# Kernel optimization log

Hardware: AMD Instinct MI355X
Metric: run time of the kernel (lower is better)

The kernel has to match this reference:

```python
import jax, jax.numpy as jnp
import numpy as np

EPS = 1e-5

def _layer_norm(x, gamma, beta):
    mu = jnp.mean(x, axis=-1, keepdims=True)
    var = jnp.var(x, axis=-1, keepdims=True)
    return (x - mu) * jax.lax.rsqrt(var + EPS) * gamma + beta

def setup_inputs() -> dict:
    key = jax.random.key(0)
    ks = jax.random.split(key, 4)
    B, T, D, H = 16, 2048, 1024, 1024
    s_in = 1.0 / np.sqrt(D)
    return {
        "x": jax.random.normal(ks[0], (B, T, D), dtype=jnp.float32),
        "c": jnp.zeros((B, H), dtype=jnp.float32),
        "W_lt": jax.random.uniform(ks[1], (H, D), jnp.float32, -s_in, s_in),
        "W_g": jax.random.uniform(ks[2], (2 * H, D), jnp.float32, -s_in, s_in),
        "b_g": jnp.zeros((2 * H,), dtype=jnp.float32),
        "gamma_g": jnp.ones((2 * H,), dtype=jnp.float32),
        "beta_g": jnp.zeros((2 * H,), dtype=jnp.float32),
        "gamma_a": jnp.ones((H,), dtype=jnp.float32),
        "beta_a": jnp.zeros((H,), dtype=jnp.float32),
    }

def reference(x, c, W_lt, W_g, b_g, gamma_g, beta_g, gamma_a, beta_a):
    H = W_lt.shape[0]
    # x: [B,T,D]
    x_tilde = jnp.einsum("btd,hd->bth", x, W_lt)            # [B,T,H]
    gate = jax.nn.sigmoid(_layer_norm(jnp.einsum("btd,gd->btg", x, W_g) + b_g, gamma_g, beta_g))
    f = gate[:, :, :H]                                        # forget gate [B,T,H]
    r = gate[:, :, H:]                                        # reset gate  [B,T,H]
    new_data = (1.0 - f) * x_tilde

    def step(c_prev, ft_nd):
        f_t, nd_t = ft_nd
        c_t = f_t * c_prev + nd_t
        return c_t, c_t

    # scan over time: move T to leading axis
    c_final, all_c = jax.lax.scan(step, c, (jnp.swapaxes(f, 0, 1), jnp.swapaxes(new_data, 0, 1)))
    all_c = jnp.swapaxes(all_c, 0, 1)                         # [B,T,H]
    h = r * jax.nn.sigmoid(_layer_norm(all_c, gamma_a, beta_a)) + (1.0 - r) * x
    return (h, c_final)
```

## Files before the change

### kernel.cpp

```cpp
#include <hip/hip_runtime.h>
#include <stdint.h>

typedef unsigned short u16;
typedef u16 us8 __attribute__((ext_vector_type(8)));
typedef uint32_t u32x8 __attribute__((ext_vector_type(8)));
typedef __bf16 bf16x8 __attribute__((ext_vector_type(8)));
typedef float f32x4 __attribute__((ext_vector_type(4)));

#define BB 16
#define TT 2048
#define HH 1024
#define MM 32768
#define NN 3072
#define KK 1024
#define NT 16

__device__ __forceinline__ float b2f(u16 u) {
    union { uint32_t i; float f; } v; v.i = ((uint32_t)u) << 16; return v.f;
}
__device__ __forceinline__ u16 f2b(float f) {
    union { uint32_t i; float f; } v; v.f = f;
    uint32_t r = v.i + 0x7fffu + ((v.i >> 16) & 1u);
    return (u16)(r >> 16);
}
__device__ __forceinline__ float sigm(float z) {
    return 1.f / (1.f + __expf(-z));
}
__device__ __forceinline__ void load_lds16(const u16* g, u16* l) {
    __builtin_amdgcn_global_load_lds(
        (const __attribute__((address_space(1))) void*)g,
        (__attribute__((address_space(3))) void*)l, 16, 0, 0);
}
__device__ __forceinline__ f32x4 mf(bf16x8 a, bf16x8 b, f32x4 c) {
    return __builtin_amdgcn_mfma_f32_16x16x32_bf16(a, b, c, 0, 0, 0);
}
#define MEMBAR() asm volatile("" ::: "memory")

__global__ __launch_bounds__(256) void k_cvt(const float* __restrict__ x,
                                             const float* __restrict__ wlt,
                                             const float* __restrict__ wg,
                                             u16* __restrict__ xb,
                                             u16* __restrict__ wb) {
    long i = (long)(blockIdx.x * 256 + threadIdx.x) * 8;
    const float* s;
    u16* o;
    if (i < 33554432L) { s = x + i; o = xb + i; }
    else {
        long j = i - 33554432L;
        s = (j < 1048576L) ? (wlt + j) : (wg + (j - 1048576L));
        o = wb + j;
    }
    float4 a = *(const float4*)(s);
    float4 b = *(const float4*)(s + 4);
    us8 r;
    r[0] = f2b(a.x); r[1] = f2b(a.y); r[2] = f2b(a.z); r[3] = f2b(a.w);
    r[4] = f2b(b.x); r[5] = f2b(b.y); r[6] = f2b(b.z); r[7] = f2b(b.w);
    *(us8*)o = r;
}

__global__ __launch_bounds__(512, 2) void k_gemm(const u16* __restrict__ A,
                                                 const u16* __restrict__ W,
                                                 u16* __restrict__ Y) {
    __shared__ u16 As[2 * 16384];
    __shared__ u16 Bs[2 * 16384];
    const int tid = threadIdx.x;
    const int lane = tid & 63;
    const int w = tid >> 6;
    const int wm = w >> 2;
    const int wn = w & 3;
    const int q = lane >> 4;
    const int l16 = lane & 15;

    const unsigned bid = blockIdx.y * 12u + blockIdx.x;
    const unsigned sw = (bid & 7u) * 192u + (bid >> 3);
    const int by = sw / 12u;
    const int bx = sw % 12u;

    const int slog = ((tid & 7) ^ ((tid >> 3) & 7)) << 3;
    const u16* aS = A + (size_t)(by * 256 + (tid >> 3)) * KK + slog;
    const u16* bS = W + (size_t)(bx * 256 + ((tid >> 8) << 6) + ((tid >> 3) & 31)) * KK + slog;
    u16* aD = As + w * 512;
    u16* bD = Bs + w * 512;

    load_lds16(aS,                aD);
    load_lds16(aS + 128 * KK,     aD + 4096);
    load_lds16(aS + 64 * KK,      aD + 8192);
    load_lds16(aS + 192 * KK,     aD + 12288);
    load_lds16(bS,                bD);
    load_lds16(bS + 128 * KK,     bD + 4096);
    load_lds16(bS + 32 * KK,      bD + 8192);
    load_lds16(bS + 160 * KK,     bD + 12288);
    load_lds16(aS + 64,           aD + 16384);
    load_lds16(aS + 64 + 128*KK,  aD + 16384 + 4096);
    load_lds16(aS + 64 + 64*KK,   aD + 16384 + 8192);
    load_lds16(aS + 64 + 192*KK,  aD + 16384 + 12288);
    load_lds16(bS + 64,           bD + 16384);
    load_lds16(bS + 64 + 128*KK,  bD + 16384 + 4096);
    load_lds16(bS + 64 + 32*KK,   bD + 16384 + 8192);
    load_lds16(bS + 64 + 160*KK,  bD + 16384 + 12288);

    const int key = l16 & 7;
    const int sA0 = ((q ^ key) << 3);
    const int sA1 = (((q ^ key) ^ 4) << 3);
    const int aB0 = wm * 4096 + l16 * 64 + sA0;
    const int aB1 = wm * 4096 + l16 * 64 + sA1;
    const int bB0 = wn * 2048 + l16 * 64 + sA0;
    const int bB1 = wn * 2048 + l16 * 64 + sA1;

    f32x4 zero = {0.f, 0.f, 0.f, 0.f};
    f32x4 acc[8][4];
#pragma unroll
    for (int i = 0; i < 8; ++i)
#pragma unroll
        for (int j = 0; j < 4; ++j) acc[i][j] = zero;
    bf16x8 aX[4], aY[4], bLo[4], bHi[4];

    asm volatile("s_waitcnt vmcnt(8)" ::: "memory");
    __builtin_amdgcn_sched_barrier(0);
    __builtin_amdgcn_s_barrier();
    MEMBAR();

    for (int kt = 0; kt < NT - 1; ++kt) {
        const int cb = (kt & 1) << 14;
        const int kc = (kt + 2) << 6;
        const bool st = (kt < NT - 2);
#pragma unroll
        for (int i = 0; i < 4; ++i) {
            aX[i] = *(const bf16x8*)&As[cb + i * 1024 + aB0];
            aY[i] = *(const bf16x8*)&As[cb + i * 1024 + aB1];
        }
        bLo[0] = *(const bf16x8*)&Bs[cb + bB0];
        bLo[1] = *(const bf16x8*)&Bs[cb + bB1];
        bLo[2] = *(const bf16x8*)&Bs[cb + 1024 + bB0];
        bLo[3] = *(const bf16x8*)&Bs[cb + 1024 + bB1];
        asm volatile("s_waitcnt lgkmcnt(8)" ::: "memory");
        __builtin_amdgcn_sched_barrier(0);
        __builtin_amdgcn_s_barrier();
        asm volatile("s_waitcnt lgkmcnt(0)" ::: "memory");
        __builtin_amdgcn_sched_barrier(0);
        __builtin_amdgcn_s_setprio(1);
#pragma unroll
        for (int i = 0; i < 4; ++i) {
            acc[i][0] = mf(aX[i], bLo[0], acc[i][0]);
            acc[i][0] = mf(aY[i], bLo[1], acc[i][0]);
            acc[i][1] = mf(aX[i], bLo[2], acc[i][1]);
            acc[i][1] = mf(aY[i], bLo[3], acc[i][1]);
        }
        __builtin_amdgcn_s_setprio(0);
        MEMBAR();
        __builtin_amdgcn_s_barrier();
        MEMBAR();
        bHi[0] = *(const bf16x8*)&Bs[cb + 8192 + bB0];
        bHi[1] = *(const bf16x8*)&Bs[cb + 8192 + bB1];
        bHi[2] = *(const bf16x8*)&Bs[cb + 8192 + 1024 + bB0];
        bHi[3] = *(const bf16x8*)&Bs[cb + 8192 + 1024 + bB1];
        if (st) {
            load_lds16(aS + kc,            aD + cb);
            load_lds16(aS + kc + 128*KK,   aD + cb + 4096);
            load_lds16(bS + kc,            bD + cb);
            load_lds16(bS + kc + 128*KK,   bD + cb + 4096);
        }
        __builtin_amdgcn_sched_barrier(0);
        __builtin_amdgcn_s_barrier();
        asm volatile("s_waitcnt lgkmcnt(0)" ::: "memory");
        __builtin_amdgcn_sched_barrier(0);
        __builtin_amdgcn_s_setprio(1);
#pragma unroll
        for (int i = 0; i < 4; ++i) {
            acc[i][2] = mf(aX[i], bHi[0], acc[i][2]);
            acc[i][2] = mf(aY[i], bHi[1], acc[i][2]);
            acc[i][3] = mf(aX[i], bHi[2], acc[i][3]);
            acc[i][3] = mf(aY[i], bHi[3], acc[i][3]);
        }
        __builtin_amdgcn_s_setprio(0);
        MEMBAR();
        __builtin_amdgcn_s_barrier();
        MEMBAR();
#pragma unroll
        for (int i = 0; i < 4; ++i) {
            aX[i] = *(const bf16x8*)&As[cb + 8192 + i * 1024 + aB0];
            aY[i] = *(const bf16x8*)&As[cb + 8192 + i * 1024 + aB1];
        }
        if (st) {
            load_lds16(bS + kc + 32*KK,    bD + cb + 8192);
            load_lds16(bS + kc + 160*KK,   bD + cb + 12288);
        }
        __builtin_amdgcn_sched_barrier(0);
        __builtin_amdgcn_s_barrier();
        asm volatile("s_waitcnt lgkmcnt(0)" ::: "memory");
        __builtin_amdgcn_sched_barrier(0);
        __builtin_amdgcn_s_setprio(1);
#pragma unroll
        for (int i = 0; i < 4; ++i) {
            acc[4 + i][0] = mf(aX[i], bLo[0], acc[4 + i][0]);
            acc[4 + i][0] = mf(aY[i], bLo[1], acc[4 + i][0]);
            acc[4 + i][1] = mf(aX[i], bLo[2], acc[4 + i][1]);
            acc[4 + i][1] = mf(aY[i], bLo[3], acc[4 + i][1]);
        }
        __builtin_amdgcn_s_setprio(0);
        MEMBAR();
        __builtin_amdgcn_s_barrier();
        MEMBAR();
        if (st) {
            load_lds16(aS + kc + 64*KK,    aD + cb + 8192);
            load_lds16(aS + kc + 192*KK,   aD + cb + 12288);
        }
        __builtin_amdgcn_sched_barrier(0);
        __builtin_amdgcn_s_barrier();
        __builtin_amdgcn_s_setprio(1);
#pragma unroll
        for (int i = 0; i < 4; ++i) {
            acc[4 + i][2] = mf(aX[i], bHi[0], acc[4 + i][2]);
            acc[4 + i][2] = mf(aY[i], bHi[1], acc[4 + i][2]);
            acc[4 + i][3] = mf(aX[i], bHi[2], acc[4 + i][3]);
            acc[4 + i][3] = mf(aY[i], bHi[3], acc[4 + i][3]);
        }
        __builtin_amdgcn_s_setprio(0);
        if (st) { asm volatile("s_waitcnt vmcnt(8)" ::: "memory"); }
        else    { asm volatile("s_waitcnt vmcnt(0)" ::: "memory"); }
        __builtin_amdgcn_sched_barrier(0);
        __builtin_amdgcn_s_barrier();
        MEMBAR();
    }

    {
        const int cb = 16384;
#pragma unroll
        for (int i = 0; i < 4; ++i) {
            aX[i] = *(const bf16x8*)&As[cb + i * 1024 + aB0];
            aY[i] = *(const bf16x8*)&As[cb + i * 1024 + aB1];
        }
        bLo[0] = *(const bf16x8*)&Bs[cb + bB0];
        bLo[1] = *(const bf16x8*)&Bs[cb + bB1];
        bLo[2] = *(const bf16x8*)&Bs[cb + 1024 + bB0];
        bLo[3] = *(const bf16x8*)&Bs[cb + 1024 + bB1];
        bHi[0] = *(const bf16x8*)&Bs[cb + 8192 + bB0];
        bHi[1] = *(const bf16x8*)&Bs[cb + 8192 + bB1];
        bHi[2] = *(const bf16x8*)&Bs[cb + 8192 + 1024 + bB0];
        bHi[3] = *(const bf16x8*)&Bs[cb + 8192 + 1024 + bB1];
#pragma unroll
        for (int i = 0; i < 4; ++i) {
            acc[i][0] = mf(aX[i], bLo[0], acc[i][0]);
            acc[i][0] = mf(aY[i], bLo[1], acc[i][0]);
            acc[i][1] = mf(aX[i], bLo[2], acc[i][1]);
            acc[i][1] = mf(aY[i], bLo[3], acc[i][1]);
            acc[i][2] = mf(aX[i], bHi[0], acc[i][2]);
            acc[i][2] = mf(aY[i], bHi[1], acc[i][2]);
            acc[i][3] = mf(aX[i], bHi[2], acc[i][3]);
            acc[i][3] = mf(aY[i], bHi[3], acc[i][3]);
        }
#pragma unroll
        for (int i = 0; i < 4; ++i) {
            aX[i] = *(const bf16x8*)&As[cb + 8192 + i * 1024 + aB0];
            aY[i] = *(const bf16x8*)&As[cb + 8192 + i * 1024 + aB1];
        }
#pragma unroll
        for (int i = 0; i < 4; ++i) {
            acc[4 + i][0] = mf(aX[i], bLo[0], acc[4 + i][0]);
            acc[4 + i][0] = mf(aY[i], bLo[1], acc[4 + i][0]);
            acc[4 + i][1] = mf(aX[i], bLo[2], acc[4 + i][1]);
            acc[4 + i][1] = mf(aY[i], bLo[3], acc[4 + i][1]);
            acc[4 + i][2] = mf(aX[i], bHi[0], acc[4 + i][2]);
            acc[4 + i][2] = mf(aY[i], bHi[1], acc[4 + i][2]);
            acc[4 + i][3] = mf(aX[i], bHi[2], acc[4 + i][3]);
            acc[4 + i][3] = mf(aY[i], bHi[3], acc[4 + i][3]);
        }
    }

#pragma unroll
    for (int fm = 0; fm < 8; ++fm) {
#pragma unroll
        for (int rg = 0; rg < 4; ++rg) {
            const int row = by * 256 + wm * 128 + fm * 16 + q * 4 + rg;
            u16* yp = Y + (size_t)row * NN + bx * 256 + wn * 64 + l16;
#pragma unroll
            for (int fn = 0; fn < 4; ++fn) yp[fn * 16] = f2b(acc[fm][fn][rg]);
        }
    }
}

__global__ __launch_bounds__(256) void k_lnsig(const u16* __restrict__ Y,
                                               const float* __restrict__ bg,
                                               const float* __restrict__ gg,
                                               const float* __restrict__ bt,
                                               uint32_t* __restrict__ FN,
                                               u16* __restrict__ R) {
    const int row = blockIdx.x;
    const int t = threadIdx.x;
    const u16* yr = Y + (size_t)row * 3072;
    us8 gv = *(const us8*)(yr + 1024 + t * 8);
    us8 xt;
    if (t < 128) xt = *(const us8*)(yr + t * 8);
    float z[8];
    float s = 0.f, s2 = 0.f;
#pragma unroll
    for (int k = 0; k < 8; k++) {
        z[k] = b2f(gv[k]) + bg[t * 8 + k];
        s += z[k];
        s2 += z[k] * z[k];
    }
#pragma unroll
    for (int m = 1; m < 64; m <<= 1) {
        s += __shfl_xor(s, m);
        s2 += __shfl_xor(s2, m);
    }
    __shared__ float red[8];
    if ((t & 63) == 0) { red[t >> 6] = s; red[(t >> 6) + 4] = s2; }
    asm volatile("s_waitcnt lgkmcnt(0)" ::: "memory");
    __builtin_amdgcn_sched_barrier(0);
    __builtin_amdgcn_s_barrier();
    MEMBAR();
    s = red[0] + red[1] + red[2] + red[3];
    s2 = red[4] + red[5] + red[6] + red[7];
    const float mu = s * (1.f / 2048.f);
    const float inv = rsqrtf(s2 * (1.f / 2048.f) - mu * mu + 1e-5f);
    float gate[8];
#pragma unroll
    for (int k = 0; k < 8; k++)
        gate[k] = sigm((z[k] - mu) * inv * gg[t * 8 + k] + bt[t * 8 + k]);
    if (t < 128) {
        u32x8 fn;
#pragma unroll
        for (int k = 0; k < 8; k++) {
            u16 fb = f2b(gate[k]);
            u16 nb = f2b((1.f - gate[k]) * b2f(xt[k]));
            fn[k] = (uint32_t)fb | ((uint32_t)nb << 16);
        }
        *(u32x8*)(FN + (size_t)row * 1024 + t * 8) = fn;
    } else {
        us8 ro;
#pragma unroll
        for (int k = 0; k < 8; k++) ro[k] = f2b(gate[k]);
        *(us8*)(R + (size_t)row * 1024 + (t - 128) * 8) = ro;
    }
}

__global__ __launch_bounds__(256) void k_scan1(const uint32_t* __restrict__ FN,
                                               float2* __restrict__ agg) {
    int u = blockIdx.x * 256 + threadIdx.x;
    int h4 = u & 255;
    int chunk = (u >> 8) & 31;
    int b = u >> 13;
    size_t base = (size_t)(b * 2048 + chunk * 64) * 1024 + h4 * 4;
    float F0 = 1.f, N0 = 0.f, F1 = 1.f, N1 = 0.f;
    float F2 = 1.f, N2 = 0.f, F3 = 1.f, N3 = 0.f;
#pragma unroll 8
    for (int i = 0; i < 64; i++) {
        uint4 v = *(const uint4*)(FN + base + (size_t)i * 1024);
        float f0 = b2f((u16)(v.x & 0xffffu)), n0 = b2f((u16)(v.x >> 16));
        float f1 = b2f((u16)(v.y & 0xffffu)), n1 = b2f((u16)(v.y >> 16));
        float f2 = b2f((u16)(v.z & 0xffffu)), n2 = b2f((u16)(v.z >> 16));
        float f3 = b2f((u16)(v.w & 0xffffu)), n3 = b2f((u16)(v.w >> 16));
        N0 = fmaf(f0, N0, n0); F0 *= f0;
        N1 = fmaf(f1, N1, n1); F1 *= f1;
        N2 = fmaf(f2, N2, n2); F2 *= f2;
        N3 = fmaf(f3, N3, n3); F3 *= f3;
    }
    size_t oi = (size_t)(b * 32 + chunk) * 1024 + h4 * 4;
    float4 oA = {F0, N0, F1, N1};
    float4 oB = {F2, N2, F3, N3};
    *(float4*)&agg[oi] = oA;
    *(float4*)&agg[oi + 2] = oB;
}

#define SOUT_STEP(fnv, rvv, xvv, ro, p)                                        \
    {                                                                          \
        c0 = fmaf(b2f((u16)((fnv).x & 0xffffu)), c0, b2f((u16)((fnv).x >> 16)));\
        c1 = fmaf(b2f((u16)((fnv).y & 0xffffu)), c1, b2f((u16)((fnv).y >> 16)));\
        float s = c0 + c1, s2 = c0 * c0 + c1 * c1;                             \
        _Pragma("unroll")                                                      \
        for (int m = 1; m < 64; m <<= 1) {                                     \
            s += __shfl_xor(s, m);                                             \
            s2 += __shfl_xor(s2, m);                                           \
        }                                                                      \
        if (lane == 0) red[p][w] = make_float2(s, s2);                         \
        asm volatile("s_waitcnt lgkmcnt(0)" ::: "memory");                     \
        __builtin_amdgcn_sched_barrier(0);                                     \
        __builtin_amdgcn_s_barrier();                                          \
        MEMBAR();                                                              \
        s = 0.f; s2 = 0.f;                                                     \
        _Pragma("unroll")                                                      \
        for (int k = 0; k < 8; k++) { float2 v = red[p][k]; s += v.x; s2 += v.y; } \
        const float mu = s * (1.f / 1024.f);                                   \
        const float inv = rsqrtf(s2 * (1.f / 1024.f) - mu * mu + 1e-5f);       \
        const float sg0 = sigm((c0 - mu) * inv * g0 + be0);                    \
        const float sg1 = sigm((c1 - mu) * inv * g1 + be1);                    \
        const float r0 = b2f((u16)((rvv) & 0xffffu)), r1 = b2f((u16)((rvv) >> 16)); \
        const float x0 = b2f((u16)((xvv) & 0xffffu)), x1 = b2f((u16)((xvv) >> 16)); \
        float2 ho = {r0 * sg0 + (1.f - r0) * x0, r1 * sg1 + (1.f - r1) * x1};  \
        *(float2*)(out + (ro)) = ho;                                           \
    }

__global__ __launch_bounds__(512) void k_scanout(const uint32_t* __restrict__ FN,
                                                 const float2* __restrict__ agg,
                                                 const float* __restrict__ cin,
                                                 const u16* __restrict__ R,
                                                 const u16* __restrict__ xb,
                                                 const float* __restrict__ ga,
                                                 const float* __restrict__ ba,
                                                 float* __restrict__ out,
                                                 float* __restrict__ cfin) {
    __shared__ float2 red[2][8];
    const int t = threadIdx.x;
    const int b = blockIdx.x >> 5, chunk = blockIdx.x & 31;
    const int h = t * 2;
    const int w = t >> 6, lane = t & 63;

    float2 cp = *(const float2*)&cin[b * 1024 + h];
    float c0 = cp.x, c1 = cp.y;
    for (int k = 0; k < chunk; ++k) {
        float4 a4 = *(const float4*)&agg[(size_t)(b * 32 + k) * 1024 + h];
        c0 = fmaf(a4.x, c0, a4.y);
        c1 = fmaf(a4.z, c1, a4.w);
    }

    const float g0 = ga[h], g1 = ga[h + 1];
    const float be0 = ba[h], be1 = ba[h + 1];
    const size_t base = (size_t)(b * 2048 + chunk * 64) * 1024 + h;

    uint2 fnA = *(const uint2*)(FN + base);
    uint32_t rvA = *(const uint32_t*)(R + base);
    uint32_t xvA = *(const uint32_t*)(xb + base);
    uint2 fnB = *(const uint2*)(FN + base + 1024);
    uint32_t rvB = *(const uint32_t*)(R + base + 1024);
    uint32_t xvB = *(const uint32_t*)(xb + base + 1024);

    for (int ii = 0; ii < 32; ++ii) {
        const size_t ro0 = base + (size_t)(2 * ii) * 1024;
        {
            uint2 fn = fnA; uint32_t rv = rvA, xv = xvA;
            if (ii < 31) {
                const size_t rn = ro0 + 2048;
                fnA = *(const uint2*)(FN + rn);
                rvA = *(const uint32_t*)(R + rn);
                xvA = *(const uint32_t*)(xb + rn);
            }
            SOUT_STEP(fn, rv, xv, ro0, 0)
        }
        {
            uint2 fn = fnB; uint32_t rv = rvB, xv = xvB;
            if (ii < 31) {
                const size_t rn = ro0 + 3072;
                fnB = *(const uint2*)(FN + rn);
                rvB = *(const uint32_t*)(R + rn);
                xvB = *(const uint32_t*)(xb + rn);
            }
            SOUT_STEP(fn, rv, xv, ro0 + 1024, 1)
        }
    }
    if (chunk == 31) *(float2*)(cfin + b * 1024 + h) = make_float2(c0, c1);
}

extern "C" void kernel_launch(void* const* d_in, const int* in_sizes, int n_in,
                              void* d_out, int out_size, void* d_ws, size_t ws_size,
                              hipStream_t stream) {
    const float* x   = (const float*)d_in[0];
    const float* c0  = (const float*)d_in[1];
    const float* wlt = (const float*)d_in[2];
    const float* wg  = (const float*)d_in[3];
    const float* bg  = (const float*)d_in[4];
    const float* gg  = (const float*)d_in[5];
    const float* btg = (const float*)d_in[6];
    const float* ga  = (const float*)d_in[7];
    const float* ba  = (const float*)d_in[8];
    float* out = (float*)d_out;

    char* ws = (char*)d_ws;
    u16* xb      = (u16*)(ws);
    u16* wb      = (u16*)(ws + 67108864);
    u16* y       = (u16*)(ws + 73400320);
    uint32_t* FN = (uint32_t*)(ws + 274726912);
    u16* R       = (u16*)(ws + 408944640);
    float2* agg  = (float2*)(ws + 476053504);

    k_cvt<<<17920, 256, 0, stream>>>(x, wlt, wg, xb, wb);
    k_gemm<<<dim3(NN / 256, MM / 256), 512, 0, stream>>>(xb, wb, y);
    k_lnsig<<<32768, 256, 0, stream>>>(y, bg, gg, btg, FN, R);
    k_scan1<<<512, 256, 0, stream>>>(FN, agg);
    k_scanout<<<512, 512, 0, stream>>>(FN, agg, c0, R, xb, ga, ba, out,
                                       out + (size_t)33554432);
}
```

Measured before the change: 634.7 us.

## Batch four timesteps per barrier in scan-output LayerNorm and vectorize gate param loads

The scan-output kernel now handles four consecutive timesteps per iteration. It interleaves their wavefront shuffle reductions and uses a single block barrier with a double-buffered shared array, where before it used one barrier per timestep. It also prefetches the next four rows of inputs. Separately, the gate LayerNorm kernel loads bias, gamma and beta as float4 vectors, replacing scalar loads. The intent is to cut barrier count and improve instruction-level parallelism, at the cost of more live registers.

```diff
diff --git a/kernel.cpp b/kernel.cpp
--- a/kernel.cpp
+++ b/kernel.cpp
@@ -291,14 +291,17 @@
     us8 gv = *(const us8*)(yr + 1024 + t * 8);
     us8 xt;
     if (t < 128) xt = *(const us8*)(yr + t * 8);
+    const float4 bgA = *(const float4*)(bg + t * 8);
+    const float4 bgB = *(const float4*)(bg + t * 8 + 4);
     float z[8];
     float s = 0.f, s2 = 0.f;
 #pragma unroll
-    for (int k = 0; k < 8; k++) {
-        z[k] = b2f(gv[k]) + bg[t * 8 + k];
-        s += z[k];
-        s2 += z[k] * z[k];
-    }
+    for (int k = 0; k < 4; k++) {
+        z[k]     = b2f(gv[k])     + ((const float*)&bgA)[k];
+        z[k + 4] = b2f(gv[k + 4]) + ((const float*)&bgB)[k];
+    }
+#pragma unroll
+    for (int k = 0; k < 8; k++) { s += z[k]; s2 = fmaf(z[k], z[k], s2); }
 #pragma unroll
     for (int m = 1; m < 64; m <<= 1) {
         s += __shfl_xor(s, m);
@@ -314,10 +317,16 @@
     s2 = red[4] + red[5] + red[6] + red[7];
     const float mu = s * (1.f / 2048.f);
     const float inv = rsqrtf(s2 * (1.f / 2048.f) - mu * mu + 1e-5f);
+    const float4 ggA = *(const float4*)(gg + t * 8);
+    const float4 ggB = *(const float4*)(gg + t * 8 + 4);
+    const float4 btA = *(const float4*)(bt + t * 8);
+    const float4 btB = *(const float4*)(bt + t * 8 + 4);
     float gate[8];
 #pragma unroll
-    for (int k = 0; k < 8; k++)
-        gate[k] = sigm((z[k] - mu) * inv * gg[t * 8 + k] + bt[t * 8 + k]);
+    for (int k = 0; k < 4; k++) {
+        gate[k]     = sigm((z[k] - mu) * inv * ((const float*)&ggA)[k] + ((const float*)&btA)[k]);
+        gate[k + 4] = sigm((z[k + 4] - mu) * inv * ((const float*)&ggB)[k] + ((const float*)&btB)[k]);
+    }
     if (t < 128) {
         u32x8 fn;
 #pragma unroll
@@ -363,34 +372,6 @@
     *(float4*)&agg[oi + 2] = oB;
 }
 
-#define SOUT_STEP(fnv, rvv, xvv, ro, p)                                        \
-    {                                                                          \
-        c0 = fmaf(b2f((u16)((fnv).x & 0xffffu)), c0, b2f((u16)((fnv).x >> 16)));\
-        c1 = fmaf(b2f((u16)((fnv).y & 0xffffu)), c1, b2f((u16)((fnv).y >> 16)));\
-        float s = c0 + c1, s2 = c0 * c0 + c1 * c1;                             \
-        _Pragma("unroll")                                                      \
-        for (int m = 1; m < 64; m <<= 1) {                                     \
-            s += __shfl_xor(s, m);                                             \
-            s2 += __shfl_xor(s2, m);                                           \
-        }                                                                      \
-        if (lane == 0) red[p][w] = make_float2(s, s2);                         \
-        asm volatile("s_waitcnt lgkmcnt(0)" ::: "memory");                     \
-        __builtin_amdgcn_sched_barrier(0);                                     \
-        __builtin_amdgcn_s_barrier();                                          \
-        MEMBAR();                                                              \
-        s = 0.f; s2 = 0.f;                                                     \
-        _Pragma("unroll")                                                      \
-        for (int k = 0; k < 8; k++) { float2 v = red[p][k]; s += v.x; s2 += v.y; } \
-        const float mu = s * (1.f / 1024.f);                                   \
-        const float inv = rsqrtf(s2 * (1.f / 1024.f) - mu * mu + 1e-5f);       \
-        const float sg0 = sigm((c0 - mu) * inv * g0 + be0);                    \
-        const float sg1 = sigm((c1 - mu) * inv * g1 + be1);                    \
-        const float r0 = b2f((u16)((rvv) & 0xffffu)), r1 = b2f((u16)((rvv) >> 16)); \
-        const float x0 = b2f((u16)((xvv) & 0xffffu)), x1 = b2f((u16)((xvv) >> 16)); \
-        float2 ho = {r0 * sg0 + (1.f - r0) * x0, r1 * sg1 + (1.f - r1) * x1};  \
-        *(float2*)(out + (ro)) = ho;                                           \
-    }
-
 __global__ __launch_bounds__(512) void k_scanout(const uint32_t* __restrict__ FN,
                                                  const float2* __restrict__ agg,
                                                  const float* __restrict__ cin,
@@ -400,7 +381,7 @@
                                                  const float* __restrict__ ba,
                                                  float* __restrict__ out,
                                                  float* __restrict__ cfin) {
-    __shared__ float2 red[2][8];
+    __shared__ float2 red[2][4][8];
     const int t = threadIdx.x;
     const int b = blockIdx.x >> 5, chunk = blockIdx.x & 31;
     const int h = t * 2;
@@ -418,35 +399,69 @@
     const float be0 = ba[h], be1 = ba[h + 1];
     const size_t base = (size_t)(b * 2048 + chunk * 64) * 1024 + h;
 
-    uint2 fnA = *(const uint2*)(FN + base);
-    uint32_t rvA = *(const uint32_t*)(R + base);
-    uint32_t xvA = *(const uint32_t*)(xb + base);
-    uint2 fnB = *(const uint2*)(FN + base + 1024);
-    uint32_t rvB = *(const uint32_t*)(R + base + 1024);
-    uint32_t xvB = *(const uint32_t*)(xb + base + 1024);
-
-    for (int ii = 0; ii < 32; ++ii) {
-        const size_t ro0 = base + (size_t)(2 * ii) * 1024;
-        {
-            uint2 fn = fnA; uint32_t rv = rvA, xv = xvA;
-            if (ii < 31) {
-                const size_t rn = ro0 + 2048;
-                fnA = *(const uint2*)(FN + rn);
-                rvA = *(const uint32_t*)(R + rn);
-                xvA = *(const uint32_t*)(xb + rn);
+    uint2 fnC[4], fnN[4];
+    uint32_t rvC[4], xvC[4], rvN[4], xvN[4];
+#pragma unroll
+    for (int s = 0; s < 4; ++s) {
+        const size_t ro = base + (size_t)s * 1024;
+        fnC[s] = *(const uint2*)(FN + ro);
+        rvC[s] = *(const uint32_t*)(R + ro);
+        xvC[s] = *(const uint32_t*)(xb + ro);
+    }
+
+    for (int bb = 0; bb < 16; ++bb) {
+        const size_t bbase = base + (size_t)(bb * 4) * 1024;
+        if (bb < 15) {
+#pragma unroll
+            for (int s = 0; s < 4; ++s) {
+                const size_t rn = bbase + (size_t)(4 + s) * 1024;
+                fnN[s] = *(const uint2*)(FN + rn);
+                rvN[s] = *(const uint32_t*)(R + rn);
+                xvN[s] = *(const uint32_t*)(xb + rn);
             }
-            SOUT_STEP(fn, rv, xv, ro0, 0)
-        }
-        {
-            uint2 fn = fnB; uint32_t rv = rvB, xv = xvB;
-            if (ii < 31) {
-                const size_t rn = ro0 + 3072;
-                fnB = *(const uint2*)(FN + rn);
-                rvB = *(const uint32_t*)(R + rn);
-                xvB = *(const uint32_t*)(xb + rn);
+        }
+        float cs0[4], cs1[4], sA[4], s2A[4];
+#pragma unroll
+        for (int s = 0; s < 4; ++s) {
+            c0 = fmaf(b2f((u16)(fnC[s].x & 0xffffu)), c0, b2f((u16)(fnC[s].x >> 16)));
+            c1 = fmaf(b2f((u16)(fnC[s].y & 0xffffu)), c1, b2f((u16)(fnC[s].y >> 16)));
+            cs0[s] = c0; cs1[s] = c1;
+            sA[s] = c0 + c1;
+            s2A[s] = c0 * c0 + c1 * c1;
+        }
+#pragma unroll
+        for (int m = 1; m < 64; m <<= 1) {
+#pragma unroll
+            for (int s = 0; s < 4; ++s) {
+                sA[s] += __shfl_xor(sA[s], m);
+                s2A[s] += __shfl_xor(s2A[s], m);
             }
-            SOUT_STEP(fn, rv, xv, ro0 + 1024, 1)
-        }
+        }
+        const int pp = bb & 1;
+        if (lane == 0) {
+#pragma unroll
+            for (int s = 0; s < 4; ++s) red[pp][s][w] = make_float2(sA[s], s2A[s]);
+        }
+        asm volatile("s_waitcnt lgkmcnt(0)" ::: "memory");
+        __builtin_amdgcn_sched_barrier(0);
+        __builtin_amdgcn_s_barrier();
+        MEMBAR();
+#pragma unroll
+        for (int s = 0; s < 4; ++s) {
+            float ss = 0.f, ss2 = 0.f;
+#pragma unroll
+            for (int k = 0; k < 8; ++k) { float2 v = red[pp][s][k]; ss += v.x; ss2 += v.y; }
+            const float mu = ss * (1.f / 1024.f);
+            const float inv = rsqrtf(ss2 * (1.f / 1024.f) - mu * mu + 1e-5f);
+            const float sg0 = sigm((cs0[s] - mu) * inv * g0 + be0);
+            const float sg1 = sigm((cs1[s] - mu) * inv * g1 + be1);
+            const float r0 = b2f((u16)(rvC[s] & 0xffffu)), r1 = b2f((u16)(rvC[s] >> 16));
+            const float x0 = b2f((u16)(xvC[s] & 0xffffu)), x1 = b2f((u16)(xvC[s] >> 16));
+            float2 ho = {r0 * sg0 + (1.f - r0) * x0, r1 * sg1 + (1.f - r1) * x1};
+            *(float2*)(out + bbase + (size_t)s * 1024) = ho;
+        }
+#pragma unroll
+        for (int s = 0; s < 4; ++s) { fnC[s] = fnN[s]; rvC[s] = rvN[s]; xvC[s] = xvN[s]; }
     }
     if (chunk == 31) *(float2*)(cfin + b * 1024 + h) = make_float2(c0, c1);
 }
```

Result: no change. 633.9 us (-0.1%).
